# Kernel tuning notes

Hardware: AMD Instinct MI355X
Metric: run time of the kernel (lower is better)

## Reference

```python
import jax, jax.numpy as jnp
import numpy as np

WIN = 2  # window half-width: window = x[b, idx-2 : idx+3]

def setup_inputs() -> dict:
    key = jax.random.key(0)
    k1, k2, k3, k4 = jax.random.split(key, 4)
    B, T, C, K, H = 64, 262144, 3, 16384, 32
    x = jax.random.normal(k1, (B, T, C), dtype=jnp.float32)
    coarse_ids = jax.random.randint(k2, (B, K), 0, T, dtype=jnp.int64)
    W1 = jax.random.normal(k3, (C, H), dtype=jnp.float32) * (1.0 / np.sqrt(C))
    b1 = jnp.zeros((H,), dtype=jnp.float32)
    W2 = jax.random.normal(k4, (H, 1), dtype=jnp.float32) * (1.0 / np.sqrt(H))
    b2 = jnp.zeros((1,), dtype=jnp.float32)
    return {"x": x, "coarse_ids": coarse_ids, "W1": W1, "b1": b1, "W2": W2, "b2": b2}

def reference(x, coarse_ids, W1, b1, W2, b2):
    B, T, C = x.shape
    K = coarse_ids.shape[1]
    offsets = jnp.arange(-WIN, WIN + 1)                    # [5]
    pos = coarse_ids[:, :, None] + offsets                 # [B,K,5]
    valid = (pos >= 0) & (pos < T)                         # boundary clipping mask
    pos_c = jnp.clip(pos, 0, T - 1)
    # batched gather of 5-point windows: [B,K,5,C]
    gathered = jnp.take_along_axis(
        x, pos_c.reshape(B, K * (2 * WIN + 1), 1), axis=1
    ).reshape(B, K, 2 * WIN + 1, C)
    vf = valid.astype(x.dtype)[..., None]                  # [B,K,5,1]
    pooled = (gathered * vf).sum(axis=2) / vf.sum(axis=2)  # masked mean -> [B,K,C]
    h = jax.nn.relu(pooled @ W1 + b1)                      # [B,K,H]
    out = (h @ W2 + b2)[..., 0]                            # [B,K]
    return out
```

## Files before the change

### kernel.cpp

```cpp
#include <hip/hip_runtime.h>
#include <hip/hip_bf16.h>

#define BB 64
#define TT 262144
#define CC 3
#define KK 16384
#define HH 32
#define WIN 2

typedef float f32x4 __attribute__((ext_vector_type(4), aligned(4)));

__device__ __forceinline__ void pool_generic(const float* __restrict__ xb, int idx,
                                             float& p0, float& p1, float& p2) {
    float s0 = 0.f, s1 = 0.f, s2 = 0.f, cnt = 0.f;
#pragma unroll
    for (int o = -WIN; o <= WIN; ++o) {
        const int pos = idx + o;
        if (pos >= 0 && pos < TT) {
            const float* p = xb + (size_t)pos * CC;
            s0 += p[0]; s1 += p[1]; s2 += p[2]; cnt += 1.f;
        }
    }
    const float rc = 1.f / cnt;
    p0 = s0 * rc; p1 = s1 * rc; p2 = s2 * rc;
}

__global__ __launch_bounds__(256) void refiner_kernel(
    const float* __restrict__ x,
    const int*   __restrict__ ids,
    const float* __restrict__ W1,
    const float* __restrict__ b1,
    const float* __restrict__ W2,
    const float* __restrict__ b2,
    float*       __restrict__ out)
{
    const int t = threadIdx.x;

    const int bid   = blockIdx.x;
    const int xcd   = bid & 7;
    const int slot  = bid >> 3;
    const int batch = ((slot >> 5) << 3) + xcd;
    const int chunk = slot & 31;
    const int pair  = batch * KK + chunk * 512 + t * 2;

    const int2 id2 = *(const int2*)(ids + pair);
    const float* __restrict__ xb = x + (size_t)batch * (size_t)TT * CC;

    float a0, a1, a2, c0, c1, c2;
    const int i0 = id2.x, i1 = id2.y;
    if (i0 >= WIN && i0 < TT - WIN && i1 >= WIN && i1 < TT - WIN) {
        const float* ba = xb + (size_t)(i0 - WIN) * CC;
        const float* bb = xb + (size_t)(i1 - WIN) * CC;
        const f32x4 A0 = *(const f32x4*)(ba);
        const f32x4 A1 = *(const f32x4*)(ba + 4);
        const f32x4 A2 = *(const f32x4*)(ba + 8);
        const f32x4 A3 = *(const f32x4*)(ba + 11);
        const f32x4 B0 = *(const f32x4*)(bb);
        const f32x4 B1 = *(const f32x4*)(bb + 4);
        const f32x4 B2 = *(const f32x4*)(bb + 8);
        const f32x4 B3 = *(const f32x4*)(bb + 11);
        a0 = (A0.x + A0.w + A1.z + A2.y + A3.y) * 0.2f;
        a1 = (A0.y + A1.x + A1.w + A2.z + A3.z) * 0.2f;
        a2 = (A0.z + A1.y + A2.x + A2.w + A3.w) * 0.2f;
        c0 = (B0.x + B0.w + B1.z + B2.y + B3.y) * 0.2f;
        c1 = (B0.y + B1.x + B1.w + B2.z + B3.z) * 0.2f;
        c2 = (B0.z + B1.y + B2.x + B2.w + B3.w) * 0.2f;
    } else {
        pool_generic(xb, i0, a0, a1, a2);
        pool_generic(xb, i1, c0, c1, c2);
    }

    float accA = b2[0];
    float accC = accA;
#pragma unroll
    for (int j = 0; j < HH; ++j) {
        const float w0 = W1[j];
        const float w1 = W1[HH + j];
        const float w2 = W1[2 * HH + j];
        const float bj = b1[j];
        const float vj = W2[j];
        float hA = fmaf(a0, w0, fmaf(a1, w1, fmaf(a2, w2, bj)));
        float hC = fmaf(c0, w0, fmaf(c1, w1, fmaf(c2, w2, bj)));
        hA = fmaxf(hA, 0.f);
        hC = fmaxf(hC, 0.f);
        accA = fmaf(hA, vj, accA);
        accC = fmaf(hC, vj, accC);
    }

    *(float2*)(out + pair) = make_float2(accA, accC);
}

extern "C" void kernel_launch(void* const* d_in, const int* in_sizes, int n_in,
                              void* d_out, int out_size, void* d_ws, size_t ws_size,
                              hipStream_t stream) {
    const float* x   = (const float*)d_in[0];
    const int*   ids = (const int*)  d_in[1];
    const float* W1  = (const float*)d_in[2];
    const float* b1  = (const float*)d_in[3];
    const float* W2  = (const float*)d_in[4];
    const float* b2  = (const float*)d_in[5];
    float* out = (float*)d_out;

    const int n = BB * KK;
    const int block = 256;
    const int grid = n / (block * 2);
    refiner_kernel<<<grid, block, 0, stream>>>(x, ids, W1, b1, W2, b2, out);
}
```

Measured before the change: 267.1 us.

## Process eight batches per thread with software-pipelined window prefetch

Each thread now handles one column across eight batches, where it previously handled two adjacent ids in one batch. All eight ids are loaded up front, and the next batch's window vectors are prefetched while the current one is pooled and run through the MLP. The grid shrinks from 2048 to 512 blocks of 256 threads, and the batches a block touches are chosen from its XCD index. This aims to hide gather latency within a thread, at the cost of fewer waves in flight and 32-bit instead of 64-bit id and output accesses.

```diff
diff --git a/kernel.cpp b/kernel.cpp
--- a/kernel.cpp
+++ b/kernel.cpp
@@ -1,5 +1,4 @@
 #include <hip/hip_runtime.h>
-#include <hip/hip_bf16.h>
 
 #define BB 64
 #define TT 262144
@@ -7,6 +6,10 @@
 #define KK 16384
 #define HH 32
 #define WIN 2
+
+#define NPHASE 8
+#define NBLK   512
+#define NT     256
 
 typedef float f32x4 __attribute__((ext_vector_type(4), aligned(4)));
 
@@ -25,7 +28,7 @@
     p0 = s0 * rc; p1 = s1 * rc; p2 = s2 * rc;
 }
 
-__global__ __launch_bounds__(256) void refiner_kernel(
+__global__ __launch_bounds__(NT) void refiner_kernel(
     const float* __restrict__ x,
     const int*   __restrict__ ids,
     const float* __restrict__ W1,
@@ -34,60 +37,70 @@
     const float* __restrict__ b2,
     float*       __restrict__ out)
 {
-    const int t = threadIdx.x;
+    const int t   = threadIdx.x;
+    const int bid = blockIdx.x;
+    const int xcd = bid & 7;
+    const int lo  = bid >> 3;
+    const int col = lo * NT + t;
 
-    const int bid   = blockIdx.x;
-    const int xcd   = bid & 7;
-    const int slot  = bid >> 3;
-    const int batch = ((slot >> 5) << 3) + xcd;
-    const int chunk = slot & 31;
-    const int pair  = batch * KK + chunk * 512 + t * 2;
+    int mid[NPHASE];
+#pragma unroll
+    for (int p = 0; p < NPHASE; ++p)
+        mid[p] = ids[(size_t)(xcd * NPHASE + p) * KK + col];
 
-    const int2 id2 = *(const int2*)(ids + pair);
-    const float* __restrict__ xb = x + (size_t)batch * (size_t)TT * CC;
-
-    float a0, a1, a2, c0, c1, c2;
-    const int i0 = id2.x, i1 = id2.y;
-    if (i0 >= WIN && i0 < TT - WIN && i1 >= WIN && i1 < TT - WIN) {
-        const float* ba = xb + (size_t)(i0 - WIN) * CC;
-        const float* bb = xb + (size_t)(i1 - WIN) * CC;
-        const f32x4 A0 = *(const f32x4*)(ba);
-        const f32x4 A1 = *(const f32x4*)(ba + 4);
-        const f32x4 A2 = *(const f32x4*)(ba + 8);
-        const f32x4 A3 = *(const f32x4*)(ba + 11);
-        const f32x4 B0 = *(const f32x4*)(bb);
-        const f32x4 B1 = *(const f32x4*)(bb + 4);
-        const f32x4 B2 = *(const f32x4*)(bb + 8);
-        const f32x4 B3 = *(const f32x4*)(bb + 11);
-        a0 = (A0.x + A0.w + A1.z + A2.y + A3.y) * 0.2f;
-        a1 = (A0.y + A1.x + A1.w + A2.z + A3.z) * 0.2f;
-        a2 = (A0.z + A1.y + A2.x + A2.w + A3.w) * 0.2f;
-        c0 = (B0.x + B0.w + B1.z + B2.y + B3.y) * 0.2f;
-        c1 = (B0.y + B1.x + B1.w + B2.z + B3.z) * 0.2f;
-        c2 = (B0.z + B1.y + B2.x + B2.w + B3.w) * 0.2f;
-    } else {
-        pool_generic(xb, i0, a0, a1, a2);
-        pool_generic(xb, i1, c0, c1, c2);
+    f32x4 a0, a1, a2, a3;
+    {
+        const int i0 = mid[0];
+        if (i0 >= WIN && i0 < TT - WIN) {
+            const float* ba = x + (size_t)(xcd * NPHASE) * TT * CC
+                                + (size_t)(i0 - WIN) * CC;
+            a0 = *(const f32x4*)(ba);
+            a1 = *(const f32x4*)(ba + 4);
+            a2 = *(const f32x4*)(ba + 8);
+            a3 = *(const f32x4*)(ba + 11);
+        }
     }
 
-    float accA = b2[0];
-    float accC = accA;
+    const float bias2 = b2[0];
+
 #pragma unroll
-    for (int j = 0; j < HH; ++j) {
-        const float w0 = W1[j];
-        const float w1 = W1[HH + j];
-        const float w2 = W1[2 * HH + j];
-        const float bj = b1[j];
-        const float vj = W2[j];
-        float hA = fmaf(a0, w0, fmaf(a1, w1, fmaf(a2, w2, bj)));
-        float hC = fmaf(c0, w0, fmaf(c1, w1, fmaf(c2, w2, bj)));
-        hA = fmaxf(hA, 0.f);
-        hC = fmaxf(hC, 0.f);
-        accA = fmaf(hA, vj, accA);
-        accC = fmaf(hC, vj, accC);
+    for (int p = 0; p < NPHASE; ++p) {
+        f32x4 n0, n1, n2, n3;
+        if (p + 1 < NPHASE) {
+            const int in = mid[p + 1];
+            if (in >= WIN && in < TT - WIN) {
+                const float* bb = x + (size_t)(xcd * NPHASE + p + 1) * TT * CC
+                                    + (size_t)(in - WIN) * CC;
+                n0 = *(const f32x4*)(bb);
+                n1 = *(const f32x4*)(bb + 4);
+                n2 = *(const f32x4*)(bb + 8);
+                n3 = *(const f32x4*)(bb + 11);
+            }
+        }
+
+        const int id = mid[p];
+        float p0, p1, p2;
+        if (id >= WIN && id < TT - WIN) {
+            p0 = (a0.x + a0.w + a1.z + a2.y + a3.y) * 0.2f;
+            p1 = (a0.y + a1.x + a1.w + a2.z + a3.z) * 0.2f;
+            p2 = (a0.z + a1.y + a2.x + a2.w + a3.w) * 0.2f;
+        } else {
+            pool_generic(x + (size_t)(xcd * NPHASE + p) * TT * CC, id, p0, p1, p2);
+        }
+
+        float acc = bias2;
+#pragma unroll
+        for (int j = 0; j < HH; ++j) {
+            float h = fmaf(p0, W1[j],
+                      fmaf(p1, W1[HH + j],
+                      fmaf(p2, W1[2 * HH + j], b1[j])));
+            acc = fmaf(fmaxf(h, 0.f), W2[j], acc);
+        }
+
+        out[(size_t)(xcd * NPHASE + p) * KK + col] = acc;
+
+        a0 = n0; a1 = n1; a2 = n2; a3 = n3;
     }
-
-    *(float2*)(out + pair) = make_float2(accA, accC);
 }
 
 extern "C" void kernel_launch(void* const* d_in, const int* in_sizes, int n_in,
@@ -101,8 +114,5 @@
     const float* b2  = (const float*)d_in[5];
     float* out = (float*)d_out;
 
-    const int n = BB * KK;
-    const int block = 256;
-    const int grid = n / (block * 2);
-    refiner_kernel<<<grid, block, 0, stream>>>(x, ids, W1, b1, W2, b2, out);
+    refiner_kernel<<<NBLK, NT, 0, stream>>>(x, ids, W1, b1, W2, b2, out);
 }
```

New measurement: 268.4 us. About the same (+0.5%).
